# Kernel tuning notes

Measured on AMD Instinct MI355X. Metric: run time of the kernel, lower is better.

The kernel has to match this reference:

```python
import jax, jax.numpy as jnp
import numpy as np

B, T, D = 2, 2048, 2048
H, HD = 16, 128
I = 5632
CAP = 0.5
EPS = 1e-6
NEG = -1e9


def _rmsnorm(x, w):
    v = x.astype(jnp.float32)
    v = v * jax.lax.rsqrt(jnp.mean(v * v, axis=-1, keepdims=True) + EPS)
    return v.astype(x.dtype) * w


def _rotate_half(x):
    x1, x2 = jnp.split(x, 2, axis=-1)
    return jnp.concatenate([-x2, x1], axis=-1)


def setup_inputs() -> dict:
    key = jax.random.key(0)
    ks = jax.random.split(key, 20)
    s = 0.02
    inp = {
        'hidden_states': jax.random.normal(ks[0], (B, T, D), jnp.float32),
        'original': jax.random.normal(ks[1], (B, T, D), jnp.float32),
        'posterior': jax.random.normal(ks[2], (B, T, D), jnp.float32),
        'prior': jax.random.normal(ks[3], (B, T, D), jnp.float32),
        'cos': jax.random.normal(ks[4], (B, T, HD), jnp.float32),
        'sin': jax.random.normal(ks[5], (B, T, HD), jnp.float32),
        'position_ids': jax.random.randint(ks[6], (B, T), 0, T),
        'q_w': jax.random.normal(ks[7], (D, H * HD), jnp.float32) * s,
        'q_b': jnp.zeros((H * HD,), jnp.float32),
        'k_w': jax.random.normal(ks[8], (D, H * HD), jnp.float32) * s,
        'k_b': jnp.zeros((H * HD,), jnp.float32),
        'v_w': jax.random.normal(ks[9], (D, H * HD), jnp.float32) * s,
        'v_b': jnp.zeros((H * HD,), jnp.float32),
        'o_w': jax.random.normal(ks[10], (H * HD, D), jnp.float32) * s,
        'ln1_w': jnp.ones((D,), jnp.float32),
        'ln2_w': jnp.ones((D,), jnp.float32),
        'gate_w': jax.random.normal(ks[11], (D, I), jnp.float32) * s,
        'up_w': jax.random.normal(ks[12], (D, I), jnp.float32) * s,
        'down_w': jax.random.normal(ks[13], (I, D), jnp.float32) * s,
        'beta_ce': jnp.array(-0.5, jnp.float32),
        'beta_cu': jnp.array(-0.8, jnp.float32),
        'ce_off': jnp.array(1.0, jnp.float32),
    }
    return inp


def reference(hidden_states, original, posterior, prior, cos, sin, position_ids,
              q_w, q_b, k_w, k_b, v_w, v_b, o_w, ln1_w, ln2_w,
              gate_w, up_w, down_w, beta_ce, beta_cu, ce_off):
    Bt, Tt, Dt = hidden_states.shape
    K = int(CAP * Tt)  # tokens selected per batch row
    # --- router: surprise scores ---
    cu = jnp.linalg.norm(original - posterior, axis=-1)  # [B,T]
    ce = jnp.linalg.norm(posterior - prior, axis=-1)     # [B,T]
    scores = beta_cu * cu + beta_ce * (ce + ce_off)      # [B,T]
    # --- capacity top-k per batch row, keep temporal order ---
    _, topi = jax.lax.top_k(scores, K)                   # [B,K]
    token_idx2 = jnp.sort(topi, axis=-1)                 # [B,K]
    sel_scores = jnp.take_along_axis(scores, token_idx2, axis=1)  # [B,K]
    b_idx = jnp.repeat(jnp.arange(Bt), K)                # [S]
    t_idx = token_idx2.reshape(-1)                       # [S]
    S = Bt * K
    sel_h = hidden_states[b_idx, t_idx]                  # [S,D]
    cos_g = cos[b_idx, t_idx][None, None]                # [1,1,S,HD]
    sin_g = sin[b_idx, t_idx][None, None]
    # --- Qwen2 decoder block on the single gathered sequence [1,S,D] ---
    x = sel_h[None]
    h = _rmsnorm(x, ln1_w)
    q = (h @ q_w + q_b).reshape(1, S, H, HD).transpose(0, 2, 1, 3)  # [1,H,S,HD]
    k = (h @ k_w + k_b).reshape(1, S, H, HD).transpose(0, 2, 1, 3)
    v = (h @ v_w + v_b).reshape(1, S, H, HD).transpose(0, 2, 1, 3)
    q = q * cos_g + _rotate_half(q) * sin_g
    k = k * cos_g + _rotate_half(k) * sin_g
    att = jnp.einsum('bhqd,bhkd->bhqk', q, k) / np.sqrt(HD)
    causal = jnp.tril(jnp.ones((S, S), bool))
    att = jnp.where(causal, att, NEG)
    att = jax.nn.softmax(att.astype(jnp.float32), axis=-1).astype(x.dtype)
    o = jnp.einsum('bhqk,bhkd->bhqd', att, v)
    o = o.transpose(0, 2, 1, 3).reshape(1, S, H * HD) @ o_w
    x = x + o
    h = _rmsnorm(x, ln2_w)
    mlp = (jax.nn.silu(h @ gate_w) * (h @ up_w)) @ down_w
    x = x + mlp
    processed = x[0]                                     # [S,D]
    # --- gated update + scatter back ---
    gate = jax.nn.sigmoid(sel_scores.reshape(-1))[:, None]
    updated = sel_h + (processed - sel_h) * gate
    output = hidden_states.at[b_idx, t_idx].set(updated)
    return output
```

## Files before the change

### kernel.cpp

```cpp
#include <hip/hip_runtime.h>


typedef unsigned short u16;
typedef unsigned int u32;
typedef short bf16x8 __attribute__((ext_vector_type(8)));
typedef float f32x4 __attribute__((ext_vector_type(4)));

#define T_LEN 2048
#define D_DIM 2048
#define B_DIM 2
#define H_NUM 16
#define HD_DIM 128
#define I_DIM 5632
#define K_CAP 1024
#define S_TOT 2048
#define QKV_N 6144
#define GU_N 11264

__device__ __forceinline__ u16 f2bf(float f) {
  union { float f; u32 u; } a; a.f = f;
  u32 r = a.u + 0x7fffu + ((a.u >> 16) & 1u);
  return (u16)(r >> 16);
}
__device__ __forceinline__ float bf2f(u16 x) {
  return __uint_as_float((u32)x << 16);
}

__device__ __forceinline__ void gld_lds16(const void* g, void* l) {
  void* gg = const_cast<void*>(g);
  __builtin_amdgcn_global_load_lds(
      (__attribute__((address_space(1))) u32*)gg,
      (__attribute__((address_space(3))) u32*)l, 16, 0, 0);
}

__global__ __launch_bounds__(256)
void router_kernel(const float* __restrict__ orig, const float* __restrict__ post,
                   const float* __restrict__ prior, const float* __restrict__ bce,
                   const float* __restrict__ bcu, const float* __restrict__ coff,
                   float* __restrict__ scores) {
  const int row = blockIdx.x;
  const size_t base = (size_t)row * D_DIM;
  float s1 = 0.f, s2 = 0.f;
  for (int d = threadIdx.x * 4; d < D_DIM; d += 1024) {
    float4 o = *(const float4*)(orig + base + d);
    float4 p = *(const float4*)(post + base + d);
    float4 r = *(const float4*)(prior + base + d);
    float a;
    a = o.x - p.x; s1 += a * a;  a = o.y - p.y; s1 += a * a;
    a = o.z - p.z; s1 += a * a;  a = o.w - p.w; s1 += a * a;
    a = p.x - r.x; s2 += a * a;  a = p.y - r.y; s2 += a * a;
    a = p.z - r.z; s2 += a * a;  a = p.w - r.w; s2 += a * a;
  }
#pragma unroll
  for (int k = 32; k; k >>= 1) { s1 += __shfl_down(s1, k); s2 += __shfl_down(s2, k); }
  __shared__ float r1[4], r2[4];
  const int wv = threadIdx.x >> 6;
  if ((threadIdx.x & 63) == 0) { r1[wv] = s1; r2[wv] = s2; }
  __syncthreads();
  if (threadIdx.x == 0) {
    float cu = sqrtf(r1[0] + r1[1] + r1[2] + r1[3]);
    float ce = sqrtf(r2[0] + r2[1] + r2[2] + r2[3]);
    scores[row] = bcu[0] * cu + bce[0] * (ce + coff[0]);
  }
}

__global__ __launch_bounds__(256)
void rank_kernel(const float* __restrict__ scores, int* __restrict__ rnk) {
  const int b = blockIdx.y;
  const int t = blockIdx.x * 256 + threadIdx.x;
  __shared__ float s[T_LEN];
  for (int u = threadIdx.x; u < T_LEN; u += 256) s[u] = scores[b * T_LEN + u];
  __syncthreads();
  const float st = s[t];
  int r = 0;
  for (int u = 0; u < T_LEN; ++u) {
    float su = s[u];
    r += ((su > st) || (su == st && u < t)) ? 1 : 0;
  }
  rnk[b * T_LEN + t] = r;
}

__global__ __launch_bounds__(256)
void compact_kernel(const float* __restrict__ scores, const int* __restrict__ rnk,
                    int* __restrict__ tidx, float* __restrict__ gate) {
  const int b = blockIdx.x;
  const int base = b * T_LEN;
  __shared__ int csum[256];
  int f[8]; int loc = 0;
  const int t0 = threadIdx.x * 8;
#pragma unroll
  for (int i = 0; i < 8; ++i) { f[i] = (rnk[base + t0 + i] < K_CAP) ? 1 : 0; loc += f[i]; }
  csum[threadIdx.x] = loc;
  __syncthreads();
  if (threadIdx.x == 0) {
    int run = 0;
    for (int i = 0; i < 256; ++i) { int tmp = csum[i]; csum[i] = run; run += tmp; }
  }
  __syncthreads();
  int pos = csum[threadIdx.x];
#pragma unroll
  for (int i = 0; i < 8; ++i) {
    if (f[i]) {
      float sc = scores[base + t0 + i];
      tidx[b * K_CAP + pos] = t0 + i;
      gate[b * K_CAP + pos] = 1.f / (1.f + __expf(-sc));
      ++pos;
    }
  }
}

__global__ __launch_bounds__(256)
void transpose_bf16_kernel(const float* __restrict__ W, u16* __restrict__ Wt,
                           int K, int N) {
  __shared__ float tile[32][33];
  const int bn = blockIdx.x * 32, bk = blockIdx.y * 32;
  const int tx = threadIdx.x & 31, ty = threadIdx.x >> 5;
#pragma unroll
  for (int i = 0; i < 32; i += 8)
    tile[ty + i][tx] = W[(size_t)(bk + ty + i) * N + bn + tx];
  __syncthreads();
#pragma unroll
  for (int i = 0; i < 32; i += 8)
    Wt[(size_t)(bn + ty + i) * K + bk + tx] = f2bf(tile[tx][ty + i]);
}

__global__ __launch_bounds__(256)
void rmsnorm_kernel(const float* __restrict__ X, const int* __restrict__ tidx,
                    const float* __restrict__ w, float* __restrict__ xcopy,
                    u16* __restrict__ Y) {
  const int s = blockIdx.x;
  const float* row;
  if (tidx) {
    const int b = s >> 10;
    const int t = tidx[s];
    row = X + ((size_t)b * T_LEN + t) * D_DIM;
  } else {
    row = X + (size_t)s * D_DIM;
  }
  const int d0 = threadIdx.x * 4;
  float4 v0 = *(const float4*)(row + d0);
  float4 v1 = *(const float4*)(row + d0 + 1024);
  float ss = v0.x*v0.x + v0.y*v0.y + v0.z*v0.z + v0.w*v0.w
           + v1.x*v1.x + v1.y*v1.y + v1.z*v1.z + v1.w*v1.w;
#pragma unroll
  for (int k = 32; k; k >>= 1) ss += __shfl_down(ss, k);
  __shared__ float red[4];
  if ((threadIdx.x & 63) == 0) red[threadIdx.x >> 6] = ss;
  __syncthreads();
  const float tot = red[0] + red[1] + red[2] + red[3];
  const float rms = rsqrtf(tot * (1.0f / D_DIM) + 1e-6f);
  if (xcopy) {
    *(float4*)(xcopy + (size_t)s * D_DIM + d0) = v0;
    *(float4*)(xcopy + (size_t)s * D_DIM + d0 + 1024) = v1;
  }
  const float4 w0 = *(const float4*)(w + d0);
  const float4 w1 = *(const float4*)(w + d0 + 1024);
  u16* yp = Y + (size_t)s * D_DIM;
  u32 a0 = (u32)f2bf(v0.x * rms * w0.x) | ((u32)f2bf(v0.y * rms * w0.y) << 16);
  u32 a1 = (u32)f2bf(v0.z * rms * w0.z) | ((u32)f2bf(v0.w * rms * w0.w) << 16);
  *(uint2*)(yp + d0) = make_uint2(a0, a1);
  u32 b0 = (u32)f2bf(v1.x * rms * w1.x) | ((u32)f2bf(v1.y * rms * w1.y) << 16);
  u32 b1 = (u32)f2bf(v1.z * rms * w1.z) | ((u32)f2bf(v1.w * rms * w1.w) << 16);
  *(uint2*)(yp + d0 + 1024) = make_uint2(b0, b1);
}

__global__ __launch_bounds__(256)
void gemm_bf16_kernel(const u16* __restrict__ A, const u16* __restrict__ Bt,
                      float* __restrict__ C, u16* __restrict__ Cbf,
                      const float* __restrict__ bias,
                      const float* __restrict__ resid, int N, int K) {
  __shared__ u16 As[128 * 32];
  __shared__ u16 Bs[128 * 32];
  const int tid = threadIdx.x;
  const int w = tid >> 6, l = tid & 63;
  const int row0 = blockIdx.y * 128, col0 = blockIdx.x * 128;
  const int wr = (w >> 1) * 64, wc = (w & 1) * 64;
  const int am = l & 15, ak = (l >> 4) * 8;
  const int srow = l >> 2, scol = (l & 3) * 8;

  f32x4 acc[4][4] = {};

  const u16* Abase = A + (size_t)(row0 + srow) * K + scol;
  const u16* Bbase = Bt + (size_t)(col0 + srow) * K + scol;
  const int R0 = (w * 2) * 16, R1 = (w * 2 + 1) * 16;

  for (int k0 = 0; k0 < K; k0 += 32) {
    gld_lds16(Abase + (size_t)R0 * K + k0, &As[R0 * 32]);
    gld_lds16(Abase + (size_t)R1 * K + k0, &As[R1 * 32]);
    gld_lds16(Bbase + (size_t)R0 * K + k0, &Bs[R0 * 32]);
    gld_lds16(Bbase + (size_t)R1 * K + k0, &Bs[R1 * 32]);
    __syncthreads();
    bf16x8 af[4], bfr[4];
#pragma unroll
    for (int i = 0; i < 4; ++i) af[i] = *(const bf16x8*)&As[(wr + i * 16 + am) * 32 + ak];
#pragma unroll
    for (int j = 0; j < 4; ++j) bfr[j] = *(const bf16x8*)&Bs[(wc + j * 16 + am) * 32 + ak];
#pragma unroll
    for (int i = 0; i < 4; ++i)
#pragma unroll
      for (int j = 0; j < 4; ++j)
        acc[i][j] = __builtin_amdgcn_mfma_f32_16x16x32_bf16(af[i], bfr[j], acc[i][j], 0, 0, 0);
    __syncthreads();
  }

  const int rb = wr + (l >> 4) * 4;
  const int cb = wc + (l & 15);
#pragma unroll
  for (int i = 0; i < 4; ++i) {
#pragma unroll
    for (int j = 0; j < 4; ++j) {
      const int colg = col0 + cb + j * 16;
      const float bv = bias ? bias[colg] : 0.0f;
#pragma unroll
      for (int r = 0; r < 4; ++r) {
        const int rowg = row0 + rb + i * 16 + r;
        const size_t idx = (size_t)rowg * N + colg;
        float v = acc[i][j][r] + bv;
        if (resid) v += resid[idx];
        if (Cbf) Cbf[idx] = f2bf(v);
        else C[idx] = v;
      }
    }
  }
}

__global__ __launch_bounds__(256)
void rope_kernel(u16* __restrict__ qkv, const float* __restrict__ cosb,
                 const float* __restrict__ sinb, const int* __restrict__ tidx) {
  const int idx = blockIdx.x * 256 + threadIdx.x;
  const int d = idx & 63;
  const int h = (idx >> 6) & 15;
  const int s = idx >> 10;
  const int b = s >> 10;
  const int t = tidx[s];
  const size_t base = (size_t)s * QKV_N + h * 128 + d;
  const size_t cb = ((size_t)b * T_LEN + t) * HD_DIM + d;
  const float c1 = cosb[cb], sn1 = sinb[cb];
  const float c2 = cosb[cb + 64], sn2 = sinb[cb + 64];
  float x1v, x2v;
  x1v = bf2f(qkv[base]); x2v = bf2f(qkv[base + 64]);
  qkv[base] = f2bf(x1v * c1 - x2v * sn1);
  qkv[base + 64] = f2bf(x2v * c2 + x1v * sn2);
  x1v = bf2f(qkv[base + 2048]); x2v = bf2f(qkv[base + 2048 + 64]);
  qkv[base + 2048] = f2bf(x1v * c1 - x2v * sn1);
  qkv[base + 2048 + 64] = f2bf(x2v * c2 + x1v * sn2);
}

__global__ __launch_bounds__(256)
void attn_mfma_kernel(const u16* __restrict__ QKV, u16* __restrict__ Og) {
  const int h = blockIdx.y;
  const int qt = 31 - (int)blockIdx.x;
  const int q0 = qt * 64;
  const int tid = threadIdx.x;
  const int w = tid >> 6, l = tid & 63;
  const int lm = l & 15, lk = l >> 4;

  __shared__ u16 Ks[64 * 136];
  __shared__ u16 Vt[128 * 72];
  __shared__ u16 Ps[64 * 72];

  const u16* Qg = QKV + h * 128;
  const u16* Kg = QKV + 2048 + h * 128;
  const u16* Vg = QKV + 4096 + h * 128;

  bf16x8 qf[4];
  {
    const u16* qrow = Qg + (size_t)(q0 + w * 16 + lm) * QKV_N;
#pragma unroll
    for (int ks = 0; ks < 4; ++ks)
      qf[ks] = *(const bf16x8*)&qrow[ks * 32 + lk * 8];
  }

  f32x4 oacc[8];
#pragma unroll
  for (int n = 0; n < 8; ++n) oacc[n] = (f32x4){0.f, 0.f, 0.f, 0.f};
  float m_run[4] = {-1e30f, -1e30f, -1e30f, -1e30f};
  float l_run[4] = {0.f, 0.f, 0.f, 0.f};

  for (int kt = 0; kt <= qt; ++kt) {
    const int kv0 = kt * 64;
    __syncthreads();
#pragma unroll
    for (int p = 0; p < 4; ++p) {
      const int i = p * 256 + tid;
      const int r = i >> 4, c8 = i & 15;
      *(uint4*)&Ks[r * 136 + c8 * 8] =
          *(const uint4*)(Kg + (size_t)(kv0 + r) * QKV_N + c8 * 8);
    }
    {
      const int d = tid >> 1;
      const int kvb = (tid & 1) * 32;
      const u16* vc = Vg + (size_t)(kv0 + kvb) * QKV_N + d;
      u16 vv[32];
#pragma unroll
      for (int j = 0; j < 32; ++j) vv[j] = vc[(size_t)j * QKV_N];
#pragma unroll
      for (int jj = 0; jj < 8; ++jj) {
        u32 lo = (u32)vv[jj * 4] | ((u32)vv[jj * 4 + 1] << 16);
        u32 hi = (u32)vv[jj * 4 + 2] | ((u32)vv[jj * 4 + 3] << 16);
        *(uint2*)&Vt[d * 72 + kvb + jj * 4] = make_uint2(lo, hi);
      }
    }
    __syncthreads();

    f32x4 sacc[4];
#pragma unroll
    for (int j = 0; j < 4; ++j) sacc[j] = (f32x4){0.f, 0.f, 0.f, 0.f};
#pragma unroll
    for (int j = 0; j < 4; ++j)
#pragma unroll
      for (int ks = 0; ks < 4; ++ks) {
        const bf16x8 kf = *(const bf16x8*)&Ks[(j * 16 + lm) * 136 + ks * 32 + lk * 8];
        sacc[j] = __builtin_amdgcn_mfma_f32_16x16x32_bf16(qf[ks], kf, sacc[j], 0, 0, 0);
      }

    const float scale = 0.08838834764831845f;
    float mx[4] = {-1e30f, -1e30f, -1e30f, -1e30f};
#pragma unroll
    for (int j = 0; j < 4; ++j) {
      const int colg = kv0 + j * 16 + lm;
#pragma unroll
      for (int r = 0; r < 4; ++r) {
        const int rowg = q0 + w * 16 + lk * 4 + r;
        float s = sacc[j][r] * scale;
        s = (colg > rowg) ? -1e30f : s;
        sacc[j][r] = s;
        mx[r] = fmaxf(mx[r], s);
      }
    }
#pragma unroll
    for (int r = 0; r < 4; ++r)
#pragma unroll
      for (int dlt = 1; dlt < 16; dlt <<= 1)
        mx[r] = fmaxf(mx[r], __shfl_xor(mx[r], dlt));
    float alpha[4];
#pragma unroll
    for (int r = 0; r < 4; ++r) {
      const float mnew = fmaxf(m_run[r], mx[r]);
      const float al = __expf(m_run[r] - mnew);
      float sum = 0.f;
#pragma unroll
      for (int j = 0; j < 4; ++j) {
        const float pe = __expf(sacc[j][r] - mnew);
        sacc[j][r] = pe;
        sum += pe;
      }
#pragma unroll
      for (int dlt = 1; dlt < 16; dlt <<= 1) sum += __shfl_xor(sum, dlt);
      l_run[r] = l_run[r] * al + sum;
      m_run[r] = mnew;
      alpha[r] = al;
    }
#pragma unroll
    for (int n = 0; n < 8; ++n)
#pragma unroll
      for (int r = 0; r < 4; ++r) oacc[n][r] *= alpha[r];

#pragma unroll
    for (int j = 0; j < 4; ++j)
#pragma unroll
      for (int r = 0; r < 4; ++r)
        Ps[(w * 16 + lk * 4 + r) * 72 + j * 16 + lm] = f2bf(sacc[j][r]);

#pragma unroll
    for (int ks2 = 0; ks2 < 2; ++ks2) {
      const bf16x8 pf = *(const bf16x8*)&Ps[(w * 16 + lm) * 72 + ks2 * 32 + lk * 8];
#pragma unroll
      for (int n = 0; n < 8; ++n) {
        const bf16x8 vf = *(const bf16x8*)&Vt[(n * 16 + lm) * 72 + ks2 * 32 + lk * 8];
        oacc[n] = __builtin_amdgcn_mfma_f32_16x16x32_bf16(pf, vf, oacc[n], 0, 0, 0);
      }
    }
  }

  float linv[4];
#pragma unroll
  for (int r = 0; r < 4; ++r) linv[r] = 1.f / l_run[r];
#pragma unroll
  for (int n = 0; n < 8; ++n)
#pragma unroll
    for (int r = 0; r < 4; ++r) {
      const int row = q0 + w * 16 + lk * 4 + r;
      Og[(size_t)row * 2048 + h * 128 + n * 16 + lm] = f2bf(oacc[n][r] * linv[r]);
    }
}

__global__ __launch_bounds__(256)
void silu_mul_kernel(const u16* __restrict__ gu, u16* __restrict__ out) {
  const size_t i = (size_t)blockIdx.x * 256 + threadIdx.x;
  const int s = (int)(i / 1408);
  const int c = (int)(i - (size_t)s * 1408);
  const uint2 g4 = *(const uint2*)&gu[(size_t)s * GU_N + c * 4];
  const uint2 u4 = *(const uint2*)&gu[(size_t)s * GU_N + I_DIM + c * 4];
  float g[4], u[4];
  g[0] = __uint_as_float(g4.x << 16); g[1] = __uint_as_float(g4.x & 0xffff0000u);
  g[2] = __uint_as_float(g4.y << 16); g[3] = __uint_as_float(g4.y & 0xffff0000u);
  u[0] = __uint_as_float(u4.x << 16); u[1] = __uint_as_float(u4.x & 0xffff0000u);
  u[2] = __uint_as_float(u4.y << 16); u[3] = __uint_as_float(u4.y & 0xffff0000u);
  u16 r[4];
#pragma unroll
  for (int j = 0; j < 4; ++j) r[j] = f2bf(g[j] * u[j] / (1.f + __expf(-g[j])));
  u32 a0 = (u32)r[0] | ((u32)r[1] << 16);
  u32 a1 = (u32)r[2] | ((u32)r[3] << 16);
  *(uint2*)&out[(size_t)s * I_DIM + c * 4] = make_uint2(a0, a1);
}

__global__ __launch_bounds__(256)
void scatter_kernel(const float* __restrict__ hs, const float* __restrict__ x2,
                    const int* __restrict__ tidx, const float* __restrict__ gate,
                    float* __restrict__ out) {
  const int s = blockIdx.x;
  const int b = s >> 10;
  const int t = tidx[s];
  const float gg = gate[s];
  const size_t src = (size_t)s * D_DIM;
  const size_t dst = ((size_t)b * T_LEN + t) * D_DIM;
  for (int d = threadIdx.x * 4; d < D_DIM; d += 1024) {
    float4 hv = *(const float4*)(hs + dst + d);
    float4 pv = *(const float4*)(x2 + src + d);
    float4 r;
    r.x = hv.x + (pv.x - hv.x) * gg;
    r.y = hv.y + (pv.y - hv.y) * gg;
    r.z = hv.z + (pv.z - hv.z) * gg;
    r.w = hv.w + (pv.w - hv.w) * gg;
    *(float4*)(out + dst + d) = r;
  }
}

extern "C" void kernel_launch(void* const* d_in, const int* in_sizes, int n_in,
                              void* d_out, int out_size, void* d_ws, size_t ws_size,
                              hipStream_t stream) {
  (void)in_sizes; (void)n_in; (void)out_size; (void)ws_size;
  const float* hs    = (const float*)d_in[0];
  const float* orig  = (const float*)d_in[1];
  const float* post  = (const float*)d_in[2];
  const float* prior = (const float*)d_in[3];
  const float* cosb  = (const float*)d_in[4];
  const float* sinb  = (const float*)d_in[5];
  const float* q_w = (const float*)d_in[7];
  const float* q_b = (const float*)d_in[8];
  const float* k_w = (const float*)d_in[9];
  const float* k_b = (const float*)d_in[10];
  const float* v_w = (const float*)d_in[11];
  const float* v_b = (const float*)d_in[12];
  const float* o_w = (const float*)d_in[13];
  const float* ln1 = (const float*)d_in[14];
  const float* ln2 = (const float*)d_in[15];
  const float* gate_w = (const float*)d_in[16];
  const float* up_w   = (const float*)d_in[17];
  const float* down_w = (const float*)d_in[18];
  const float* beta_ce = (const float*)d_in[19];
  const float* beta_cu = (const float*)d_in[20];
  const float* ce_off  = (const float*)d_in[21];
  float* out = (float*)d_out;

  char* wsp = (char*)d_ws;
  size_t off = 0;
  auto alloc = [&](size_t n) -> char* {
    char* r = wsp + off; off += (n + 255) & ~(size_t)255; return r;
  };
  const size_t SD4 = (size_t)S_TOT * D_DIM * 4;

  float* scores  = (float*)alloc((size_t)B_DIM * T_LEN * 4);
  int*   rnk     = (int*)  alloc((size_t)B_DIM * T_LEN * 4);
  int*   tidx    = (int*)  alloc((size_t)S_TOT * 4);
  float* gatebuf = (float*)alloc((size_t)S_TOT * 4);
  float* qkvbias = (float*)alloc((size_t)QKV_N * 4);
  u16* qkvwt = (u16*)alloc((size_t)QKV_N * 2048 * 2);
  u16* owt   = (u16*)alloc((size_t)2048 * 2048 * 2);
  u16* guwt  = (u16*)alloc((size_t)GU_N * 2048 * 2);
  u16* dwt   = (u16*)alloc((size_t)2048 * I_DIM * 2);
  char* rA = alloc(SD4);
  float* selh = (float*)rA;
  u16*   h2   = (u16*)rA;
  char* rB = alloc((size_t)S_TOT * I_DIM * 2);
  u16* h1     = (u16*)rB;
  u16* o_attn = (u16*)rB;
  u16* mlp_in = (u16*)rB;
  char* rC = alloc((size_t)S_TOT * GU_N * 2);
  u16* qkv_bf = (u16*)rC;
  u16* gu_bf  = (u16*)rC;
  float* x2   = (float*)rC;
  float* x1 = (float*)alloc(SD4);

  hipMemcpyAsync(out, hs, (size_t)B_DIM * T_LEN * D_DIM * 4,
                 hipMemcpyDeviceToDevice, stream);
  hipMemcpyAsync(qkvbias, q_b, 2048 * 4, hipMemcpyDeviceToDevice, stream);
  hipMemcpyAsync(qkvbias + 2048, k_b, 2048 * 4, hipMemcpyDeviceToDevice, stream);
  hipMemcpyAsync(qkvbias + 4096, v_b, 2048 * 4, hipMemcpyDeviceToDevice, stream);

  router_kernel<<<dim3(B_DIM * T_LEN), 256, 0, stream>>>(orig, post, prior,
                                                         beta_ce, beta_cu, ce_off, scores);
  rank_kernel<<<dim3(8, B_DIM), 256, 0, stream>>>(scores, rnk);
  compact_kernel<<<dim3(B_DIM), 256, 0, stream>>>(scores, rnk, tidx, gatebuf);

  transpose_bf16_kernel<<<dim3(64, 64), 256, 0, stream>>>(q_w, qkvwt, 2048, 2048);
  transpose_bf16_kernel<<<dim3(64, 64), 256, 0, stream>>>(k_w, qkvwt + (size_t)2048 * 2048, 2048, 2048);
  transpose_bf16_kernel<<<dim3(64, 64), 256, 0, stream>>>(v_w, qkvwt + (size_t)4096 * 2048, 2048, 2048);
  transpose_bf16_kernel<<<dim3(64, 64), 256, 0, stream>>>(o_w, owt, 2048, 2048);
  transpose_bf16_kernel<<<dim3(176, 64), 256, 0, stream>>>(gate_w, guwt, 2048, I_DIM);
  transpose_bf16_kernel<<<dim3(176, 64), 256, 0, stream>>>(up_w, guwt + (size_t)I_DIM * 2048, 2048, I_DIM);
  transpose_bf16_kernel<<<dim3(64, 176), 256, 0, stream>>>(down_w, dwt, I_DIM, 2048);

  rmsnorm_kernel<<<dim3(S_TOT), 256, 0, stream>>>(hs, tidx, ln1, selh, h1);

  gemm_bf16_kernel<<<dim3(48, 16), 256, 0, stream>>>(h1, qkvwt, nullptr, qkv_bf,
                                                     qkvbias, nullptr, QKV_N, 2048);
  rope_kernel<<<dim3((S_TOT * H_NUM * 64) / 256), 256, 0, stream>>>(qkv_bf, cosb, sinb, tidx);

  attn_mfma_kernel<<<dim3(32, H_NUM), 256, 0, stream>>>(qkv_bf, o_attn);

  gemm_bf16_kernel<<<dim3(16, 16), 256, 0, stream>>>(o_attn, owt, x1, nullptr,
                                                     nullptr, selh, 2048, 2048);

  rmsnorm_kernel<<<dim3(S_TOT), 256, 0, stream>>>(x1, nullptr, ln2, nullptr, h2);

  gemm_bf16_kernel<<<dim3(88, 16), 256, 0, stream>>>(h2, guwt, nullptr, gu_bf,
                                                     nullptr, nullptr, GU_N, 2048);

  silu_mul_kernel<<<dim3((S_TOT * (I_DIM / 4)) / 256), 256, 0, stream>>>(gu_bf, mlp_in);

  gemm_bf16_kernel<<<dim3(16, 16), 256, 0, stream>>>(mlp_in, dwt, x2, nullptr,
                                                     nullptr, x1, 2048, I_DIM);

  scatter_kernel<<<dim3(S_TOT), 256, 0, stream>>>(hs, x2, tidx, gatebuf, out);
}
```

Before: 1.083 ms.

## Split attention KV tiles across two warp groups with pre-transposed V and swizzled LDS

Adds a kernel that transposes V into a head-major buffer ahead of attention. The attention kernel now runs 512 threads, and two 4-wave groups handle alternating KV tiles for the same query tile, with a final merge of their softmax states through shared memory. K and V tiles are loaded with direct global-to-LDS copies into XOR-swizzled layouts, replacing the strided scalar V gather and the padded layouts. The query-tile order alternates by head to balance the causal workload. The cost is an extra transpose kernel, more barriers per iteration, a merge epilogue, and 64KB of shared memory per block, which limits occupancy.

```diff
diff --git a/kernel.cpp b/kernel.cpp
--- a/kernel.cpp
+++ b/kernel.cpp
@@ -122,6 +122,21 @@
 #pragma unroll
   for (int i = 0; i < 32; i += 8)
     Wt[(size_t)(bn + ty + i) * K + bk + tx] = f2bf(tile[tx][ty + i]);
+}
+
+__global__ __launch_bounds__(256)
+void vtrans_kernel(const u16* __restrict__ qkv, u16* __restrict__ VT) {
+  __shared__ u16 tile[32][34];
+  const int s0 = blockIdx.x * 32;
+  const int c0 = blockIdx.y * 32;
+  const int tx = threadIdx.x & 31, ty = threadIdx.x >> 5;
+#pragma unroll
+  for (int i = 0; i < 32; i += 8)
+    tile[ty + i][tx] = qkv[(size_t)(s0 + ty + i) * QKV_N + 4096 + c0 + tx];
+  __syncthreads();
+#pragma unroll
+  for (int i = 0; i < 32; i += 8)
+    VT[(size_t)(c0 + ty + i) * S_TOT + s0 + tx] = tile[tx][ty + i];
 }
 
 __global__ __launch_bounds__(256)
@@ -246,29 +261,44 @@
   qkv[base + 2048 + 64] = f2bf(x2v * c2 + x1v * sn2);
 }
 
-__global__ __launch_bounds__(256)
-void attn_mfma_kernel(const u16* __restrict__ QKV, u16* __restrict__ Og) {
-  const int h = blockIdx.y;
-  const int qt = 31 - (int)blockIdx.x;
+__global__ __launch_bounds__(512, 4)
+void attn_mfma_kernel(const u16* __restrict__ QKV, const u16* __restrict__ VT,
+                      u16* __restrict__ Og) {
+  const int h  = blockIdx.y;
+  const int bx = blockIdx.x;
+  const int qt = (h < 8) ? (31 - bx) : bx;
   const int q0 = qt * 64;
   const int tid = threadIdx.x;
-  const int w = tid >> 6, l = tid & 63;
+  const int l  = tid & 63;
+  const int w  = tid >> 6;
+  const int g  = w >> 2;
+  const int wq = w & 3;
   const int lm = l & 15, lk = l >> 4;
 
-  __shared__ u16 Ks[64 * 136];
-  __shared__ u16 Vt[128 * 72];
-  __shared__ u16 Ps[64 * 72];
-
-  const u16* Qg = QKV + h * 128;
-  const u16* Kg = QKV + 2048 + h * 128;
-  const u16* Vg = QKV + 4096 + h * 128;
+  __shared__ __align__(16) unsigned char smem[65536];
+  u16* Ks = (u16*)(smem + g * 16384);
+  u16* Vt = (u16*)(smem + 32768 + g * 16384);
+  u16* Ps = (u16*)(smem + g * 16384);
+
+  const u16* Qg  = QKV + h * 128;
+  const u16* Kg  = QKV + 2048 + h * 128;
+  const u16* Vgt = VT + (size_t)h * 128 * S_TOT;
 
   bf16x8 qf[4];
   {
-    const u16* qrow = Qg + (size_t)(q0 + w * 16 + lm) * QKV_N;
-#pragma unroll
-    for (int ks = 0; ks < 4; ++ks)
-      qf[ks] = *(const bf16x8*)&qrow[ks * 32 + lk * 8];
+    const u16* qrow = Qg + (size_t)(q0 + wq * 16 + lm) * QKV_N;
+#pragma unroll
+    for (int ks = 0; ks < 4; ++ks) qf[ks] = *(const bf16x8*)&qrow[ks * 32 + lk * 8];
+  }
+
+  int ksrc[4], vsrc[4];
+#pragma unroll
+  for (int p = 0; p < 4; ++p) {
+    const int ci = (wq * 4 + p) * 64 + l;
+    const int kr = ci >> 4, kc = ci & 15;
+    ksrc[p] = kr * QKV_N + ((kc ^ (kr & 7)) * 8);
+    const int vr = ci >> 3, vc = ci & 7;
+    vsrc[p] = vr * S_TOT + ((vc ^ (vr & 7)) * 8);
   }
 
   f32x4 oacc[8];
@@ -277,112 +307,146 @@
   float m_run[4] = {-1e30f, -1e30f, -1e30f, -1e30f};
   float l_run[4] = {0.f, 0.f, 0.f, 0.f};
 
-  for (int kt = 0; kt <= qt; ++kt) {
+  const int ntiles = (g == 0) ? (qt / 2 + 1) : ((qt + 1) / 2);
+  const int nmax = qt / 2 + 1;
+  const float scale = 0.08838834764831845f;
+
+  for (int it = 0; it < nmax; ++it) {
+    const int kt = g + 2 * it;
     const int kv0 = kt * 64;
+    const bool active = (it < ntiles);
     __syncthreads();
-#pragma unroll
-    for (int p = 0; p < 4; ++p) {
-      const int i = p * 256 + tid;
-      const int r = i >> 4, c8 = i & 15;
-      *(uint4*)&Ks[r * 136 + c8 * 8] =
-          *(const uint4*)(Kg + (size_t)(kv0 + r) * QKV_N + c8 * 8);
-    }
-    {
-      const int d = tid >> 1;
-      const int kvb = (tid & 1) * 32;
-      const u16* vc = Vg + (size_t)(kv0 + kvb) * QKV_N + d;
-      u16 vv[32];
-#pragma unroll
-      for (int j = 0; j < 32; ++j) vv[j] = vc[(size_t)j * QKV_N];
-#pragma unroll
-      for (int jj = 0; jj < 8; ++jj) {
-        u32 lo = (u32)vv[jj * 4] | ((u32)vv[jj * 4 + 1] << 16);
-        u32 hi = (u32)vv[jj * 4 + 2] | ((u32)vv[jj * 4 + 3] << 16);
-        *(uint2*)&Vt[d * 72 + kvb + jj * 4] = make_uint2(lo, hi);
+    if (active) {
+#pragma unroll
+      for (int p = 0; p < 4; ++p) {
+        gld_lds16(Kg + (size_t)kv0 * QKV_N + ksrc[p], &Ks[(wq * 4 + p) * 512]);
+        gld_lds16(Vgt + kv0 + vsrc[p],               &Vt[(wq * 4 + p) * 512]);
       }
     }
     __syncthreads();
 
     f32x4 sacc[4];
-#pragma unroll
-    for (int j = 0; j < 4; ++j) sacc[j] = (f32x4){0.f, 0.f, 0.f, 0.f};
-#pragma unroll
-    for (int j = 0; j < 4; ++j)
-#pragma unroll
-      for (int ks = 0; ks < 4; ++ks) {
-        const bf16x8 kf = *(const bf16x8*)&Ks[(j * 16 + lm) * 136 + ks * 32 + lk * 8];
-        sacc[j] = __builtin_amdgcn_mfma_f32_16x16x32_bf16(qf[ks], kf, sacc[j], 0, 0, 0);
-      }
-
-    const float scale = 0.08838834764831845f;
-    float mx[4] = {-1e30f, -1e30f, -1e30f, -1e30f};
-#pragma unroll
-    for (int j = 0; j < 4; ++j) {
-      const int colg = kv0 + j * 16 + lm;
+    if (active) {
+#pragma unroll
+      for (int j = 0; j < 4; ++j) sacc[j] = (f32x4){0.f, 0.f, 0.f, 0.f};
+#pragma unroll
+      for (int j = 0; j < 4; ++j) {
+        const int row = j * 16 + lm;
+#pragma unroll
+        for (int ks = 0; ks < 4; ++ks) {
+          const int c = ks * 4 + lk;
+          const bf16x8 kf = *(const bf16x8*)&(
+              (const unsigned char*)Ks)[row * 256 + ((c ^ (row & 7)) << 4)];
+          sacc[j] = __builtin_amdgcn_mfma_f32_16x16x32_bf16(qf[ks], kf, sacc[j], 0, 0, 0);
+        }
+      }
+    }
+    __syncthreads();
+
+    if (active) {
+      float mx[4] = {-1e30f, -1e30f, -1e30f, -1e30f};
+#pragma unroll
+      for (int j = 0; j < 4; ++j) {
+        const int colg = kv0 + j * 16 + lm;
+#pragma unroll
+        for (int r = 0; r < 4; ++r) {
+          const int rowg = q0 + wq * 16 + lk * 4 + r;
+          float s = sacc[j][r] * scale;
+          s = (colg > rowg) ? -1e30f : s;
+          sacc[j][r] = s;
+          mx[r] = fmaxf(mx[r], s);
+        }
+      }
+#pragma unroll
+      for (int r = 0; r < 4; ++r)
+#pragma unroll
+        for (int dlt = 1; dlt < 16; dlt <<= 1)
+          mx[r] = fmaxf(mx[r], __shfl_xor(mx[r], dlt));
+      float alpha[4];
 #pragma unroll
       for (int r = 0; r < 4; ++r) {
-        const int rowg = q0 + w * 16 + lk * 4 + r;
-        float s = sacc[j][r] * scale;
-        s = (colg > rowg) ? -1e30f : s;
-        sacc[j][r] = s;
-        mx[r] = fmaxf(mx[r], s);
-      }
-    }
-#pragma unroll
-    for (int r = 0; r < 4; ++r)
-#pragma unroll
-      for (int dlt = 1; dlt < 16; dlt <<= 1)
-        mx[r] = fmaxf(mx[r], __shfl_xor(mx[r], dlt));
-    float alpha[4];
+        const float mnew = fmaxf(m_run[r], mx[r]);
+        const float al = __expf(m_run[r] - mnew);
+        float sum = 0.f;
+#pragma unroll
+        for (int j = 0; j < 4; ++j) {
+          const float pe = __expf(sacc[j][r] - mnew);
+          sacc[j][r] = pe;
+          sum += pe;
+        }
+#pragma unroll
+        for (int dlt = 1; dlt < 16; dlt <<= 1) sum += __shfl_xor(sum, dlt);
+        l_run[r] = l_run[r] * al + sum;
+        m_run[r] = mnew;
+        alpha[r] = al;
+      }
+#pragma unroll
+      for (int n = 0; n < 8; ++n)
+#pragma unroll
+        for (int r = 0; r < 4; ++r) oacc[n][r] *= alpha[r];
+
+#pragma unroll
+      for (int j = 0; j < 4; ++j)
+#pragma unroll
+        for (int r = 0; r < 4; ++r) {
+          const int row = wq * 16 + lk * 4 + r;
+          *(u16*)&((unsigned char*)Ps)[row * 128 +
+              (((j * 16 + lm) * 2) ^ ((row & 7) << 4))] = f2bf(sacc[j][r]);
+        }
+
+#pragma unroll
+      for (int ks2 = 0; ks2 < 2; ++ks2) {
+        const int prow = wq * 16 + lm;
+        const bf16x8 pf = *(const bf16x8*)&(
+            (const unsigned char*)Ps)[prow * 128 +
+                ((ks2 * 64 + lk * 16) ^ ((prow & 7) << 4))];
+#pragma unroll
+        for (int n = 0; n < 8; ++n) {
+          const int vrow = n * 16 + lm;
+          const int vc = ks2 * 4 + lk;
+          const bf16x8 vf = *(const bf16x8*)&(
+              (const unsigned char*)Vt)[vrow * 128 + ((vc ^ (vrow & 7)) << 4)];
+          oacc[n] = __builtin_amdgcn_mfma_f32_16x16x32_bf16(pf, vf, oacc[n], 0, 0, 0);
+        }
+      }
+    }
+  }
+
+  __syncthreads();
+  float* Obuf = (float*)smem;
+  float* Mbuf = (float*)(smem + 33792);
+  float* Lbuf = (float*)(smem + 34048);
+  if (g == 1) {
 #pragma unroll
     for (int r = 0; r < 4; ++r) {
-      const float mnew = fmaxf(m_run[r], mx[r]);
-      const float al = __expf(m_run[r] - mnew);
-      float sum = 0.f;
-#pragma unroll
-      for (int j = 0; j < 4; ++j) {
-        const float pe = __expf(sacc[j][r] - mnew);
-        sacc[j][r] = pe;
-        sum += pe;
-      }
-#pragma unroll
-      for (int dlt = 1; dlt < 16; dlt <<= 1) sum += __shfl_xor(sum, dlt);
-      l_run[r] = l_run[r] * al + sum;
-      m_run[r] = mnew;
-      alpha[r] = al;
+      const int row = wq * 16 + lk * 4 + r;
+      if (lm == 0) { Mbuf[row] = m_run[r]; Lbuf[row] = l_run[r]; }
+#pragma unroll
+      for (int n = 0; n < 8; ++n) Obuf[row * 132 + n * 16 + lm] = oacc[n][r];
+    }
+  }
+  __syncthreads();
+  if (g == 0) {
+    float a0[4], a1[4], linv[4];
+#pragma unroll
+    for (int r = 0; r < 4; ++r) {
+      const int row = wq * 16 + lk * 4 + r;
+      const float m1 = Mbuf[row], l1 = Lbuf[row];
+      const float M = fmaxf(m_run[r], m1);
+      a0[r] = __expf(m_run[r] - M);
+      a1[r] = __expf(m1 - M);
+      linv[r] = 1.f / (a0[r] * l_run[r] + a1[r] * l1);
     }
 #pragma unroll
     for (int n = 0; n < 8; ++n)
 #pragma unroll
-      for (int r = 0; r < 4; ++r) oacc[n][r] *= alpha[r];
-
-#pragma unroll
-    for (int j = 0; j < 4; ++j)
-#pragma unroll
-      for (int r = 0; r < 4; ++r)
-        Ps[(w * 16 + lk * 4 + r) * 72 + j * 16 + lm] = f2bf(sacc[j][r]);
-
-#pragma unroll
-    for (int ks2 = 0; ks2 < 2; ++ks2) {
-      const bf16x8 pf = *(const bf16x8*)&Ps[(w * 16 + lm) * 72 + ks2 * 32 + lk * 8];
-#pragma unroll
-      for (int n = 0; n < 8; ++n) {
-        const bf16x8 vf = *(const bf16x8*)&Vt[(n * 16 + lm) * 72 + ks2 * 32 + lk * 8];
-        oacc[n] = __builtin_amdgcn_mfma_f32_16x16x32_bf16(pf, vf, oacc[n], 0, 0, 0);
-      }
-    }
-  }
-
-  float linv[4];
-#pragma unroll
-  for (int r = 0; r < 4; ++r) linv[r] = 1.f / l_run[r];
-#pragma unroll
-  for (int n = 0; n < 8; ++n)
-#pragma unroll
-    for (int r = 0; r < 4; ++r) {
-      const int row = q0 + w * 16 + lk * 4 + r;
-      Og[(size_t)row * 2048 + h * 128 + n * 16 + lm] = f2bf(oacc[n][r] * linv[r]);
-    }
+      for (int r = 0; r < 4; ++r) {
+        const int row = wq * 16 + lk * 4 + r;
+        const float o = (oacc[n][r] * a0[r] +
+                         Obuf[row * 132 + n * 16 + lm] * a1[r]) * linv[r];
+        Og[(size_t)(q0 + row) * 2048 + h * 128 + n * 16 + lm] = f2bf(o);
+      }
+  }
 }
 
 __global__ __launch_bounds__(256)
@@ -482,6 +546,7 @@
   u16* gu_bf  = (u16*)rC;
   float* x2   = (float*)rC;
   float* x1 = (float*)alloc(SD4);
+  u16* vT = (u16*)x1;
 
   hipMemcpyAsync(out, hs, (size_t)B_DIM * T_LEN * D_DIM * 4,
                  hipMemcpyDeviceToDevice, stream);
@@ -508,7 +573,9 @@
                                                      qkvbias, nullptr, QKV_N, 2048);
   rope_kernel<<<dim3((S_TOT * H_NUM * 64) / 256), 256, 0, stream>>>(qkv_bf, cosb, sinb, tidx);
 
-  attn_mfma_kernel<<<dim3(32, H_NUM), 256, 0, stream>>>(qkv_bf, o_attn);
+  vtrans_kernel<<<dim3(64, 64), 256, 0, stream>>>(qkv_bf, vT);
+
+  attn_mfma_kernel<<<dim3(32, H_NUM), 512, 0, stream>>>(qkv_bf, vT, o_attn);
 
   gemm_bf16_kernel<<<dim3(16, 16), 256, 0, stream>>>(o_attn, owt, x1, nullptr,
                                                      nullptr, selh, 2048, 2048);
```

Measured after the change: 996.6 us. -8.0%, faster.
